# Performance work log

Measured on AMD Instinct MI355X. Metric: run time of the kernel, lower is better.

## Reference

```python
import jax, jax.numpy as jnp
import numpy as np

LEAK = 0.1   # LeakyReLU negative slope used by Conv2dBatchLeaky
EPS = 1e-5   # BatchNorm eps (torch default)


def conv_bn_leaky(x, w, gamma, beta, mean, var, stride, pad):
    # Conv2d(bias=False) -> BatchNorm (inference) -> LeakyReLU(0.1)
    y = jax.lax.conv_general_dilated(
        x, w, (stride, stride), [(pad, pad), (pad, pad)],
        dimension_numbers=("NCHW", "OIHW", "NCHW"))
    scale = gamma / jnp.sqrt(var + EPS)
    shift = beta - mean * scale
    y = y * scale[None, :, None, None] + shift[None, :, None, None]
    return jnp.where(y > 0, y, LEAK * y)


def reorg(x, s):
    # lightnet Reorg: exact permutation of the darknet reorg layer
    B, C, H, W = x.shape
    x = x.reshape(B, C, H // s, s, W // s, s)
    x = x.transpose(0, 3, 5, 1, 2, 4)           # (B, s, s, C, H/s, W/s)
    return x.reshape(B, s * s * C, H // s, W // s)


def setup_inputs() -> dict:
    key = jax.random.key(0)
    ks = jax.random.split(key, 13)
    B = 64
    inp = {
        "feat0": jax.random.normal(ks[0], (B, 1024, 19, 19), jnp.float32),
        "feat1": jax.random.normal(ks[1], (B, 512, 38, 38), jnp.float32),
        "w1": jax.random.normal(ks[2], (64, 512, 1, 1), jnp.float32) * 0.05,
        "g1": jax.random.uniform(ks[3], (64,), jnp.float32, 0.5, 1.5),
        "b1": jax.random.normal(ks[4], (64,), jnp.float32) * 0.1,
        "m1": jax.random.normal(ks[5], (64,), jnp.float32) * 0.1,
        "v1": jax.random.uniform(ks[6], (64,), jnp.float32, 0.5, 1.5),
        "w2": jax.random.normal(ks[7], (1024, 1280, 3, 3), jnp.float32) * 0.02,
        "g2": jax.random.uniform(ks[8], (1024,), jnp.float32, 0.5, 1.5),
        "b2": jax.random.normal(ks[9], (1024,), jnp.float32) * 0.1,
        "m2": jax.random.normal(ks[10], (1024,), jnp.float32) * 0.1,
        "v2": jax.random.uniform(ks[11], (1024,), jnp.float32, 0.5, 1.5),
        # meta_state: (num_classes=20, num_anchors*6=30, 1024+1)
        "reweight": jax.random.normal(ks[12], (20, 30, 1025), jnp.float32) * 0.05,
    }
    return inp


def reference(feat0, feat1, w1, g1, b1, m1, v1, w2, g2, b2, m2, v2, reweight):
    # layers[0]: 1x1 ConvBatchLeaky(512->64) + Reorg(2)
    x = conv_bn_leaky(feat1, w1, g1, b1, m1, v1, stride=1, pad=0)
    x = reorg(x, 2)                                  # (B, 256, 19, 19)
    # layers[1]: 3x3 ConvBatchLeaky(1280->1024), pad=1
    cat = jnp.concatenate([x, feat0], axis=1)        # (B, 1280, 19, 19)
    pre = conv_bn_leaky(cat, w2, g2, b2, m2, v2, stride=1, pad=1)  # (B,1024,19,19)
    # get_reweighted_output: per-class dynamic 1x1 conv, batched as one einsum
    cw = reweight[:, :, :-1]                         # (K=20, O=30, 1024)
    cb = reweight[:, :, -1]                          # (K, O)
    det = jnp.einsum("bchw,koc->bkohw", pre, cw) + cb[None, :, :, None, None]
    B, _, _, H, W = det.shape
    return det.reshape(B * 20, 30, H, W)
```

## Files before the change

### kernel.cpp

```cpp
#include <hip/hip_runtime.h>

typedef unsigned short u16;
typedef __attribute__((ext_vector_type(8))) __bf16 bf16x8;
typedef __attribute__((ext_vector_type(4))) float f32x4;

__device__ __forceinline__ u16 f2bf(float f) {
  union { float f; unsigned u; } v; v.f = f;
  unsigned r = v.u + 0x7fffu + ((v.u >> 16) & 1u);
  return (u16)(r >> 16);
}

__device__ __forceinline__ void gld16(const void* g, const void* l) {
  __builtin_amdgcn_global_load_lds((const __attribute__((address_space(1))) void*)g,
                                   (__attribute__((address_space(3))) void*)l, 16, 0, 0);
}

__global__ __launch_bounds__(256) void k_prep_small(
    const float* w1, const float* rw,
    const float* g1, const float* b1, const float* m1, const float* v1,
    const float* g2, const float* b2, const float* m2, const float* v2,
    u16* w1b, u16* cwt,
    float* scale1, float* shift1, float* scale2, float* shift2, float* cbf)
{
  int i = blockIdx.x * 256 + threadIdx.x;
  if (i < 32768) { w1b[i] = f2bf(w1[i]); return; }
  i -= 32768;
  if (i < 655360) {
    int n = i >> 10, c = i & 1023;
    cwt[i] = (n < 600) ? f2bf(rw[n * 1025 + c]) : (u16)0;
    return;
  }
  i -= 655360;
  if (i < 64) {
    float s = g1[i] * rsqrtf(v1[i] + 1e-5f);
    scale1[i] = s; shift1[i] = b1[i] - m1[i] * s;
  } else if (i < 1088) {
    int c = i - 64;
    float s = g2[c] * rsqrtf(v2[c] + 1e-5f);
    scale2[c] = s; shift2[c] = b2[c] - m2[c] * s;
  } else if (i < 1728) {
    int n = i - 1088;
    cbf[n] = (n < 600) ? rw[n * 1025 + 1024] : 0.f;
  }
}

__global__ __launch_bounds__(256) void k_prep_w2(const float* w2, u16* w2t) {
  __shared__ float buf[11520];
  int o = blockIdx.x;
  const float* src = w2 + (size_t)o * 11520;
  for (int i = threadIdx.x; i < 11520; i += 256) buf[i] = src[i];
  __syncthreads();
  for (int t = 0; t < 9; ++t) {
    int dy = t / 3, dx = t - dy * 3;
    u16* dst = w2t + ((size_t)dy * 1024 + o) * 3840 + dx * 1280;
    for (int ci = threadIdx.x; ci < 1280; ci += 256) dst[ci] = f2bf(buf[ci * 9 + t]);
  }
}

__global__ __launch_bounds__(256) void k_feat0(const float* feat0, u16* cat) {
  __shared__ float tile[32][33];
  int b = blockIdx.z, c0 = blockIdx.y * 32, p0 = blockIdx.x * 32;
  int tid = threadIdx.x;
  int lo = tid & 31, hi = tid >> 5;
#pragma unroll
  for (int pass = 0; pass < 4; ++pass) {
    int cl = pass * 8 + hi;
    int p = p0 + lo;
    tile[cl][lo] = (p < 361) ? feat0[((size_t)(b * 1024 + c0 + cl)) * 361 + p] : 0.f;
  }
  __syncthreads();
#pragma unroll
  for (int pass = 0; pass < 4; ++pass) {
    int pl = pass * 8 + hi;
    int p = p0 + pl;
    if (p < 361) {
      int h = p / 19, w = p - h * 19;
      cat[(((size_t)b * 21 + 1 + h) * 21 + 1 + w) * 1280 + 256 + c0 + lo] = f2bf(tile[lo][pl]);
    }
  }
}

__global__ __launch_bounds__(256) void k_conv1(const float* feat1, const u16* w1b,
    const float* scale1, const float* shift1, u16* cat)
{
  __shared__ u16 As[128 * 40];
  __shared__ u16 Bs[64 * 32];
  int tid = threadIdx.x;
  int wave = tid >> 6, lane = tid & 63;
  int wr = wave >> 1, wc = wave & 1;
  int lm = lane & 15, lq = lane >> 4;
  int csw = (lq ^ ((lm >> 1) & 3)) * 8;
  int m0 = blockIdx.x * 128;

  int mLoc = tid & 127, cHalf = tid >> 7;
  int mA = m0 + mLoc;
  int bA = mA / 1444, qA = mA - bA * 1444;
  const float* aG = feat1 + ((size_t)bA * 512) * 1444 + qA;

  const u16* bG = w1b + (tid >> 2) * 512 + (((tid & 3) ^ ((tid >> 3) & 3)) * 8);
  char* BsW = (char*)Bs + wave * 1024;

  f32x4 acc[4][2];
#pragma unroll
  for (int i = 0; i < 4; ++i)
#pragma unroll
    for (int j = 0; j < 2; ++j)
#pragma unroll
      for (int r = 0; r < 4; ++r) acc[i][j][r] = 0.f;

  for (int k0 = 0; k0 < 512; k0 += 32) {
    gld16(bG + k0, BsW);
#pragma unroll
    for (int pass = 0; pass < 16; ++pass) {
      int c = pass * 2 + cHalf;
      As[mLoc * 40 + c] = f2bf(aG[(size_t)(k0 + c) * 1444]);
    }
    __syncthreads();
    bf16x8 aF[4], bF[2];
#pragma unroll
    for (int i = 0; i < 4; ++i)
      aF[i] = *(const bf16x8*)(As + (wr * 64 + i * 16 + lm) * 40 + lq * 8);
#pragma unroll
    for (int j = 0; j < 2; ++j)
      bF[j] = *(const bf16x8*)(Bs + (wc * 32 + j * 16 + lm) * 32 + csw);
#pragma unroll
    for (int i = 0; i < 4; ++i)
#pragma unroll
      for (int j = 0; j < 2; ++j)
        acc[i][j] = __builtin_amdgcn_mfma_f32_16x16x32_bf16(aF[i], bF[j], acc[i][j], 0, 0, 0);
    __syncthreads();
  }

  int o0 = wc * 32;
  float sc[2], sh[2];
#pragma unroll
  for (int j = 0; j < 2; ++j) {
    int o = o0 + j * 16 + lm;
    sc[j] = scale1[o]; sh[j] = shift1[o];
  }
#pragma unroll
  for (int i = 0; i < 4; ++i) {
#pragma unroll
    for (int r = 0; r < 4; ++r) {
      int m = m0 + wr * 64 + i * 16 + lq * 4 + r;
      int b = m / 1444, q = m - b * 1444;
      int yy = q / 38, xx = q - yy * 38;
      size_t base = (((size_t)b * 21 + 1 + (yy >> 1)) * 21 + 1 + (xx >> 1)) * 1280
                  + ((yy & 1) * 2 + (xx & 1)) * 64;
#pragma unroll
      for (int j = 0; j < 2; ++j) {
        float v = acc[i][j][r] * sc[j] + sh[j];
        v = v > 0.f ? v : 0.1f * v;
        cat[base + o0 + j * 16 + lm] = f2bf(v);
      }
    }
  }
}

__global__ __launch_bounds__(256) void k_conv2(const u16* cat, const u16* w2t,
    const float* scale2, const float* shift2, u16* pre)
{
  __shared__ u16 As[8192];
  __shared__ u16 Bs[8192];
  int tid = threadIdx.x;
  int wave = tid >> 6, lane = tid & 63;
  int wr = wave >> 1, wc = wave & 1;
  int lm = lane & 15, lq = lane >> 4;
  int csw = (lq ^ ((lm >> 1) & 3)) * 8;
  int n0 = (blockIdx.x & 7) * 128;
  int m0 = (blockIdx.x >> 3) * 128;

  int rIn = lane >> 2;
  int kseg = (((lane & 3) ^ ((lane >> 3) & 3)) * 8);
  int rowLo = wave * 16 + rIn;

  int mLo = m0 + rowLo;       if (mLo > 23103) mLo = 23103;
  int mHi = m0 + rowLo + 64;  if (mHi > 23103) mHi = 23103;
  int bL = mLo / 361, pL = mLo - bL * 361, yL = pL / 19, xL = pL - yL * 19;
  int bH = mHi / 361, pH = mHi - bH * 361, yH = pH / 19, xH = pH - yH * 19;
  const u16* aLo = cat + ((size_t)(bL * 21 + yL) * 21 + xL) * 1280 + kseg;
  const u16* aHi = cat + ((size_t)(bH * 21 + yH) * 21 + xH) * 1280 + kseg;
  const u16* bLo = w2t + (size_t)(n0 + rowLo) * 3840 + kseg;
  const u16* bHi = bLo + (size_t)64 * 3840;

  u16* asJ0 = As + wave * 512;          u16* asJ1 = As + (4 + wave) * 512;
  u16* asJ2 = As + 4096 + wave * 512;   u16* asJ3 = As + 4096 + (4 + wave) * 512;
  u16* bsJ0 = Bs + wave * 512;          u16* bsJ1 = Bs + (4 + wave) * 512;
  u16* bsJ2 = Bs + 4096 + wave * 512;   u16* bsJ3 = Bs + 4096 + (4 + wave) * 512;

  f32x4 acc[4][4];
#pragma unroll
  for (int i = 0; i < 4; ++i)
#pragma unroll
    for (int j = 0; j < 4; ++j)
#pragma unroll
      for (int r = 0; r < 4; ++r) acc[i][j][r] = 0.f;

  for (int dy = 0; dy < 3; ++dy) {
    const u16* a0 = aLo + dy * 26880;
    const u16* a1 = aHi + dy * 26880;
    const u16* b0 = bLo + (size_t)dy * 3932160;
    const u16* b1 = bHi + (size_t)dy * 3932160;
    for (int k0 = 0; k0 < 3840; k0 += 64) {
      gld16(a0 + k0,      asJ0);
      gld16(a1 + k0,      asJ1);
      gld16(a0 + k0 + 32, asJ2);
      gld16(a1 + k0 + 32, asJ3);
      gld16(b0 + k0,      bsJ0);
      gld16(b1 + k0,      bsJ1);
      gld16(b0 + k0 + 32, bsJ2);
      gld16(b1 + k0 + 32, bsJ3);
      __syncthreads();
#pragma unroll
      for (int kk = 0; kk < 2; ++kk) {
        bf16x8 aF[4], bF[4];
#pragma unroll
        for (int i = 0; i < 4; ++i)
          aF[i] = *(const bf16x8*)(As + kk * 4096 + (wr * 64 + i * 16 + lm) * 32 + csw);
#pragma unroll
        for (int j = 0; j < 4; ++j)
          bF[j] = *(const bf16x8*)(Bs + kk * 4096 + (wc * 64 + j * 16 + lm) * 32 + csw);
#pragma unroll
        for (int i = 0; i < 4; ++i)
#pragma unroll
          for (int j = 0; j < 4; ++j)
            acc[i][j] = __builtin_amdgcn_mfma_f32_16x16x32_bf16(aF[i], bF[j], acc[i][j], 0, 0, 0);
      }
      __syncthreads();
    }
  }

  int nn[4]; float sc[4], sh[4];
#pragma unroll
  for (int j = 0; j < 4; ++j) {
    nn[j] = n0 + wc * 64 + j * 16 + lm;
    sc[j] = scale2[nn[j]]; sh[j] = shift2[nn[j]];
  }
#pragma unroll
  for (int i = 0; i < 4; ++i) {
#pragma unroll
    for (int r = 0; r < 4; ++r) {
      int m = m0 + wr * 64 + i * 16 + lq * 4 + r;
      if (m < 23104) {
        u16* row = pre + (size_t)m * 1024;
#pragma unroll
        for (int j = 0; j < 4; ++j) {
          float v = acc[i][j][r] * sc[j] + sh[j];
          v = v > 0.f ? v : 0.1f * v;
          row[nn[j]] = f2bf(v);
        }
      }
    }
  }
}

__global__ __launch_bounds__(256) void k_einsum(const u16* pre, const u16* cwt,
    const float* cbf, float* out)
{
  __shared__ u16 As[4096];
  __shared__ u16 Bs[4096];
  int tid = threadIdx.x;
  int wave = tid >> 6, lane = tid & 63;
  int wr = wave >> 1, wc = wave & 1;
  int lm = lane & 15, lq = lane >> 4;
  int csw = (lq ^ ((lm >> 1) & 3)) * 8;
  int m0 = blockIdx.x * 128;
  int n0 = blockIdx.y * 128;

  int r0 = tid >> 2;
  int seg = (((tid & 3) ^ ((tid >> 3) & 3)) * 8);
  const u16* aP0 = cwt + (size_t)(m0 + r0) * 1024 + seg;
  const u16* aP1 = aP0 + (size_t)64 * 1024;
  int q0 = n0 + r0;       if (q0 > 23103) q0 = 23103;
  int q1 = n0 + r0 + 64;  if (q1 > 23103) q1 = 23103;
  const u16* bP0 = pre + (size_t)q0 * 1024 + seg;
  const u16* bP1 = pre + (size_t)q1 * 1024 + seg;

  char* AsW = (char*)As + wave * 1024;
  char* BsW = (char*)Bs + wave * 1024;

  f32x4 acc[4][4];
#pragma unroll
  for (int i = 0; i < 4; ++i)
#pragma unroll
    for (int j = 0; j < 4; ++j)
#pragma unroll
      for (int r = 0; r < 4; ++r) acc[i][j][r] = 0.f;

  for (int k0 = 0; k0 < 1024; k0 += 32) {
    gld16(aP0 + k0, AsW);
    gld16(aP1 + k0, AsW + 4096);
    gld16(bP0 + k0, BsW);
    gld16(bP1 + k0, BsW + 4096);
    __syncthreads();
    bf16x8 aF[4], bF[4];
#pragma unroll
    for (int i = 0; i < 4; ++i)
      aF[i] = *(const bf16x8*)(As + (wr * 64 + i * 16 + lm) * 32 + csw);
#pragma unroll
    for (int j = 0; j < 4; ++j)
      bF[j] = *(const bf16x8*)(Bs + (wc * 64 + j * 16 + lm) * 32 + csw);
#pragma unroll
    for (int i = 0; i < 4; ++i)
#pragma unroll
      for (int j = 0; j < 4; ++j)
        acc[i][j] = __builtin_amdgcn_mfma_f32_16x16x32_bf16(aF[i], bF[j], acc[i][j], 0, 0, 0);
    __syncthreads();
  }

  int pix[4], pb[4], pp[4];
#pragma unroll
  for (int j = 0; j < 4; ++j) {
    pix[j] = n0 + wc * 64 + j * 16 + lm;
    int b = pix[j] / 361;
    pb[j] = b; pp[j] = pix[j] - b * 361;
  }
#pragma unroll
  for (int i = 0; i < 4; ++i) {
#pragma unroll
    for (int r = 0; r < 4; ++r) {
      int cw = m0 + wr * 64 + i * 16 + lq * 4 + r;
      if (cw < 600) {
        float bias = cbf[cw];
#pragma unroll
        for (int j = 0; j < 4; ++j) {
          if (pix[j] < 23104)
            out[(size_t)pb[j] * 216600 + (size_t)cw * 361 + pp[j]] = acc[i][j][r] + bias;
        }
      }
    }
  }
}


extern "C" void kernel_launch(void* const* d_in, const int* in_sizes, int n_in,
                              void* d_out, int out_size, void* d_ws, size_t ws_size,
                              hipStream_t stream) {
  const float* feat0 = (const float*)d_in[0];
  const float* feat1 = (const float*)d_in[1];
  const float* w1 = (const float*)d_in[2];
  const float* g1 = (const float*)d_in[3];
  const float* b1 = (const float*)d_in[4];
  const float* m1 = (const float*)d_in[5];
  const float* v1 = (const float*)d_in[6];
  const float* w2 = (const float*)d_in[7];
  const float* g2 = (const float*)d_in[8];
  const float* b2 = (const float*)d_in[9];
  const float* m2 = (const float*)d_in[10];
  const float* v2 = (const float*)d_in[11];
  const float* rw = (const float*)d_in[12];
  float* out = (float*)d_out;

  char* ws = (char*)d_ws;
  u16* cat    = (u16*)(ws);
  u16* w2t    = (u16*)(ws + 72253440);
  u16* pre    = (u16*)(ws + 95846400);
  u16* w1b    = (u16*)(ws + 143163392);
  u16* cwt    = (u16*)(ws + 143228928);
  float* scale1 = (float*)(ws + 144539648);
  float* shift1 = (float*)(ws + 144539904);
  float* scale2 = (float*)(ws + 144540160);
  float* shift2 = (float*)(ws + 144544256);
  float* cbf    = (float*)(ws + 144548352);

  hipMemsetAsync(cat, 0, 72253440, stream);

  k_prep_small<<<2696, 256, 0, stream>>>(w1, rw, g1, b1, m1, v1, g2, b2, m2, v2,
                                         w1b, cwt, scale1, shift1, scale2, shift2, cbf);
  k_prep_w2<<<1024, 256, 0, stream>>>(w2, w2t);
  k_feat0<<<dim3(12, 32, 64), 256, 0, stream>>>(feat0, cat);
  k_conv1<<<722, 256, 0, stream>>>(feat1, w1b, scale1, shift1, cat);
  k_conv2<<<1448, 256, 0, stream>>>(cat, w2t, scale2, shift2, pre);
  k_einsum<<<dim3(5, 181), 256, 0, stream>>>(pre, cwt, cbf, out);
}
```

Measured before the change: 1.189 ms.

## Rewrite conv2 GEMM as 256x256-tile, 8-wave, double-buffered pipelined kernel

The main implicit-GEMM conv kernel moves from 128x128 tiles with 4 waves to 256x256 tiles with 8 waves. Each wave now holds 128x64 accumulators. LDS is double-buffered with 64-wide K slices and uses an XOR swizzle. Global-to-LDS loads for the next stage are interleaved between four MFMA phases, using explicit vmcnt/lgkmcnt waits, barriers and s_setprio so memory traffic overlaps compute. The intent is to raise arithmetic intensity and hide load latency. In exchange it needs far more registers and 128KB of LDS, and launches only 364 blocks, which risks tail imbalance on 256 CUs.

Result: slower. 1.219 ms (+2.5%).

```diff
diff --git a/kernel.cpp b/kernel.cpp
--- a/kernel.cpp
+++ b/kernel.cpp
@@ -14,6 +14,13 @@
   __builtin_amdgcn_global_load_lds((const __attribute__((address_space(1))) void*)g,
                                    (__attribute__((address_space(3))) void*)l, 16, 0, 0);
 }
+
+#define BARX() do { asm volatile("" ::: "memory"); __builtin_amdgcn_s_barrier(); \
+                    asm volatile("" ::: "memory"); } while (0)
+#define LGKM0() do { asm volatile("s_waitcnt lgkmcnt(0)" ::: "memory"); \
+                     __builtin_amdgcn_sched_barrier(0); } while (0)
+#define VMC(n) do { asm volatile("s_waitcnt vmcnt(" #n ")" ::: "memory"); \
+                    __builtin_amdgcn_sched_barrier(0); } while (0)
 
 __global__ __launch_bounds__(256) void k_prep_small(
     const float* w1, const float* rw,
@@ -157,77 +164,155 @@
   }
 }
 
-__global__ __launch_bounds__(256) void k_conv2(const u16* cat, const u16* w2t,
+__global__ __launch_bounds__(512, 2) void k_conv2(const u16* cat, const u16* w2t,
     const float* scale2, const float* shift2, u16* pre)
 {
-  __shared__ u16 As[8192];
-  __shared__ u16 Bs[8192];
-  int tid = threadIdx.x;
-  int wave = tid >> 6, lane = tid & 63;
-  int wr = wave >> 1, wc = wave & 1;
-  int lm = lane & 15, lq = lane >> 4;
-  int csw = (lq ^ ((lm >> 1) & 3)) * 8;
-  int n0 = (blockIdx.x & 7) * 128;
-  int m0 = (blockIdx.x >> 3) * 128;
-
-  int rIn = lane >> 2;
-  int kseg = (((lane & 3) ^ ((lane >> 3) & 3)) * 8);
-  int rowLo = wave * 16 + rIn;
-
-  int mLo = m0 + rowLo;       if (mLo > 23103) mLo = 23103;
-  int mHi = m0 + rowLo + 64;  if (mHi > 23103) mHi = 23103;
-  int bL = mLo / 361, pL = mLo - bL * 361, yL = pL / 19, xL = pL - yL * 19;
-  int bH = mHi / 361, pH = mHi - bH * 361, yH = pH / 19, xH = pH - yH * 19;
-  const u16* aLo = cat + ((size_t)(bL * 21 + yL) * 21 + xL) * 1280 + kseg;
-  const u16* aHi = cat + ((size_t)(bH * 21 + yH) * 21 + xH) * 1280 + kseg;
-  const u16* bLo = w2t + (size_t)(n0 + rowLo) * 3840 + kseg;
-  const u16* bHi = bLo + (size_t)64 * 3840;
-
-  u16* asJ0 = As + wave * 512;          u16* asJ1 = As + (4 + wave) * 512;
-  u16* asJ2 = As + 4096 + wave * 512;   u16* asJ3 = As + 4096 + (4 + wave) * 512;
-  u16* bsJ0 = Bs + wave * 512;          u16* bsJ1 = Bs + (4 + wave) * 512;
-  u16* bsJ2 = Bs + 4096 + wave * 512;   u16* bsJ3 = Bs + 4096 + (4 + wave) * 512;
-
-  f32x4 acc[4][4];
-#pragma unroll
-  for (int i = 0; i < 4; ++i)
+  __shared__ __align__(16) u16 As[2][16384];
+  __shared__ __align__(16) u16 Bs[2][16384];
+
+  const int tid = threadIdx.x;
+  const int wave = tid >> 6, lane = tid & 63;
+  const int wr = wave >> 2, wc = wave & 3;
+  const int lm = lane & 15, lq = lane >> 4;
+  const int m0 = (blockIdx.x >> 2) * 256;
+  const int n0 = (blockIdx.x & 3) * 256;
+
+  const int rsub = tid >> 3;
+  const int cOff = ((tid & 7) ^ ((tid >> 4) & 7)) * 8;
+  const int ldsT = rsub * 64 + (tid & 7) * 8;
+
+  const u16* aBase[4];
+#pragma unroll
+  for (int q = 0; q < 4; ++q) {
+    int m = m0 + q * 64 + rsub; if (m > 23103) m = 23103;
+    int b = m / 361, pq = m - b * 361, y = pq / 19, x = pq - y * 19;
+    aBase[q] = cat + ((size_t)(b * 21 + y) * 21 + x) * 1280 + cOff;
+  }
+  const u16* bBase[4];
+#pragma unroll
+  for (int q = 0; q < 4; ++q)
+    bBase[q] = w2t + (size_t)(n0 + q * 64 + rsub) * 3840 + cOff;
+
+  int ck[2];
+#pragma unroll
+  for (int ks = 0; ks < 2; ++ks) ck[ks] = ((ks * 4 + lq) ^ ((lm >> 1) & 7)) * 8;
+
+  f32x4 acc[8][4];
+#pragma unroll
+  for (int i = 0; i < 8; ++i)
 #pragma unroll
     for (int j = 0; j < 4; ++j)
 #pragma unroll
       for (int r = 0; r < 4; ++r) acc[i][j][r] = 0.f;
 
-  for (int dy = 0; dy < 3; ++dy) {
-    const u16* a0 = aLo + dy * 26880;
-    const u16* a1 = aHi + dy * 26880;
-    const u16* b0 = bLo + (size_t)dy * 3932160;
-    const u16* b1 = bHi + (size_t)dy * 3932160;
-    for (int k0 = 0; k0 < 3840; k0 += 64) {
-      gld16(a0 + k0,      asJ0);
-      gld16(a1 + k0,      asJ1);
-      gld16(a0 + k0 + 32, asJ2);
-      gld16(a1 + k0 + 32, asJ3);
-      gld16(b0 + k0,      bsJ0);
-      gld16(b1 + k0,      bsJ1);
-      gld16(b0 + k0 + 32, bsJ2);
-      gld16(b1 + k0 + 32, bsJ3);
-      __syncthreads();
-#pragma unroll
-      for (int kk = 0; kk < 2; ++kk) {
-        bf16x8 aF[4], bF[4];
-#pragma unroll
-        for (int i = 0; i < 4; ++i)
-          aF[i] = *(const bf16x8*)(As + kk * 4096 + (wr * 64 + i * 16 + lm) * 32 + csw);
-#pragma unroll
-        for (int j = 0; j < 4; ++j)
-          bF[j] = *(const bf16x8*)(Bs + kk * 4096 + (wc * 64 + j * 16 + lm) * 32 + csw);
-#pragma unroll
-        for (int i = 0; i < 4; ++i)
-#pragma unroll
-          for (int j = 0; j < 4; ++j)
-            acc[i][j] = __builtin_amdgcn_mfma_f32_16x16x32_bf16(aF[i], bF[j], acc[i][j], 0, 0, 0);
-      }
-      __syncthreads();
-    }
+  auto stA = [&](int p, int part, int off) {
+#pragma unroll
+    for (int s = 0; s < 2; ++s) {
+      int q = s * 2 + part;
+      gld16(aBase[q] + off, &As[p][q * 4096 + ldsT]);
+    }
+  };
+  auto stB = [&](int p, int g, int off) {
+#pragma unroll
+    for (int s = 0; s < 2; ++s) {
+      int q = g * 2 + s;
+      gld16(bBase[q] + off, &Bs[p][q * 4096 + ldsT]);
+    }
+  };
+
+  stA(0, 0, 0);  stB(0, 0, 0);  stA(0, 1, 0);  stB(0, 1, 0);
+  stA(1, 0, 64); stB(1, 0, 64); stA(1, 1, 64); stB(1, 1, 64);
+  VMC(8);
+  BARX();
+
+  int dyS = 0, koS = 128;
+
+  for (int kt = 0; kt < 180; ++kt) {
+    const int p = kt & 1;
+    const bool pf = (kt < 178);
+    const int offA = dyS * 26880 + koS;
+    const int offB = dyS * 3932160 + koS;
+    const u16* Ap = &As[p][(wr * 128 + lm) * 64];
+    const u16* Bp = &Bs[p][(wc * 64 + lm) * 64];
+
+    bf16x8 aF[4][2], bF[4][2];
+
+#pragma unroll
+    for (int i = 0; i < 4; ++i)
+#pragma unroll
+      for (int ks = 0; ks < 2; ++ks)
+        aF[i][ks] = *(const bf16x8*)(Ap + i * 1024 + ck[ks]);
+#pragma unroll
+    for (int j = 0; j < 2; ++j)
+#pragma unroll
+      for (int ks = 0; ks < 2; ++ks)
+        bF[j][ks] = *(const bf16x8*)(Bp + j * 1024 + ck[ks]);
+    BARX();
+    LGKM0();
+    __builtin_amdgcn_s_setprio(1);
+#pragma unroll
+    for (int ks = 0; ks < 2; ++ks)
+#pragma unroll
+      for (int i = 0; i < 4; ++i)
+#pragma unroll
+        for (int j = 0; j < 2; ++j)
+          acc[i][j] = __builtin_amdgcn_mfma_f32_16x16x32_bf16(aF[i][ks], bF[j][ks], acc[i][j], 0, 0, 0);
+    __builtin_amdgcn_s_setprio(0);
+    BARX();
+
+#pragma unroll
+    for (int j = 2; j < 4; ++j)
+#pragma unroll
+      for (int ks = 0; ks < 2; ++ks)
+        bF[j][ks] = *(const bf16x8*)(Bp + j * 1024 + ck[ks]);
+    if (pf) stA(p, 0, offA);
+    BARX();
+    LGKM0();
+    __builtin_amdgcn_s_setprio(1);
+#pragma unroll
+    for (int ks = 0; ks < 2; ++ks)
+#pragma unroll
+      for (int i = 0; i < 4; ++i)
+#pragma unroll
+        for (int j = 2; j < 4; ++j)
+          acc[i][j] = __builtin_amdgcn_mfma_f32_16x16x32_bf16(aF[i][ks], bF[j][ks], acc[i][j], 0, 0, 0);
+    __builtin_amdgcn_s_setprio(0);
+    if (pf) { VMC(12); } else { VMC(0); }
+    BARX();
+
+#pragma unroll
+    for (int i = 0; i < 4; ++i)
+#pragma unroll
+      for (int ks = 0; ks < 2; ++ks)
+        aF[i][ks] = *(const bf16x8*)(Ap + 4096 + i * 1024 + ck[ks]);
+    if (pf) stB(p, 0, offB);
+    BARX();
+    LGKM0();
+    __builtin_amdgcn_s_setprio(1);
+#pragma unroll
+    for (int ks = 0; ks < 2; ++ks)
+#pragma unroll
+      for (int i = 0; i < 4; ++i)
+#pragma unroll
+        for (int j = 2; j < 4; ++j)
+          acc[4 + i][j] = __builtin_amdgcn_mfma_f32_16x16x32_bf16(aF[i][ks], bF[j][ks], acc[4 + i][j], 0, 0, 0);
+    __builtin_amdgcn_s_setprio(0);
+    BARX();
+
+    if (pf) { stA(p, 1, offA); stB(p, 1, offB); }
+    __builtin_amdgcn_s_setprio(1);
+#pragma unroll
+    for (int ks = 0; ks < 2; ++ks)
+#pragma unroll
+      for (int i = 0; i < 4; ++i)
+#pragma unroll
+        for (int j = 0; j < 2; ++j)
+          acc[4 + i][j] = __builtin_amdgcn_mfma_f32_16x16x32_bf16(aF[i][ks], bF[j][ks], acc[4 + i][j], 0, 0, 0);
+    __builtin_amdgcn_s_setprio(0);
+    if (pf) { VMC(8); } else { VMC(0); }
+    BARX();
+
+    koS += 64; if (koS == 3840) { koS = 0; ++dyS; }
   }
 
   int nn[4]; float sc[4], sh[4];
@@ -237,10 +322,10 @@
     sc[j] = scale2[nn[j]]; sh[j] = shift2[nn[j]];
   }
 #pragma unroll
-  for (int i = 0; i < 4; ++i) {
+  for (int i = 0; i < 8; ++i) {
 #pragma unroll
     for (int r = 0; r < 4; ++r) {
-      int m = m0 + wr * 64 + i * 16 + lq * 4 + r;
+      int m = m0 + wr * 128 + i * 16 + lq * 4 + r;
       if (m < 23104) {
         u16* row = pre + (size_t)m * 1024;
 #pragma unroll
@@ -370,6 +455,6 @@
   k_prep_w2<<<1024, 256, 0, stream>>>(w2, w2t);
   k_feat0<<<dim3(12, 32, 64), 256, 0, stream>>>(feat0, cat);
   k_conv1<<<722, 256, 0, stream>>>(feat1, w1b, scale1, shift1, cat);
-  k_conv2<<<1448, 256, 0, stream>>>(cat, w2t, scale2, shift2, pre);
+  k_conv2<<<364, 512, 0, stream>>>(cat, w2t, scale2, shift2, pre);
   k_einsum<<<dim3(5, 181), 256, 0, stream>>>(pre, cwt, cbf, out);
 }
```
